# Kernel tuning notes

Hardware: AMD Instinct MI355X
Metric: run time of the kernel (lower is better)

Reference implementation:

```python
import jax, jax.numpy as jnp
import numpy as np

HIDDEN = 2048
NUM_HEADS = 32
NUM_KV_HEADS = 8
HEAD_DIM = 128
EPS = 1e-6
ROPE_BASE = 10000.0
T = 2048


def setup_inputs() -> dict:
    key = jax.random.key(0)
    k1, k2, k3, k4, k5 = jax.random.split(key, 5)
    q_size = NUM_HEADS * HEAD_DIM
    kv_size = NUM_KV_HEADS * HEAD_DIM
    s = 0.02
    return {
        "positions": jnp.arange(T, dtype=jnp.int32),
        "hidden_states": jax.random.normal(k1, (T, HIDDEN), dtype=jnp.float32),
        "wqkv": jax.random.normal(k2, (q_size + 2 * kv_size, HIDDEN), dtype=jnp.float32) * s,
        "wo": jax.random.normal(k3, (HIDDEN, q_size), dtype=jnp.float32) * s,
        "q_norm_w": jnp.ones((HEAD_DIM,), dtype=jnp.float32),
        "k_norm_w": jnp.ones((HEAD_DIM,), dtype=jnp.float32),
    }


def _rms_norm(x, w, eps=EPS):
    # x: [T, H, D]; normalize over last dim
    var = jnp.mean(jnp.square(x), axis=-1, keepdims=True)
    return x * jax.lax.rsqrt(var + eps) * w


def _rope(positions, x):
    # neox-style rotate-half RoPE. x: [T, H, D]
    half = HEAD_DIM // 2
    inv_freq = 1.0 / (ROPE_BASE ** (jnp.arange(0, half, dtype=jnp.float32) / half))
    ang = positions.astype(jnp.float32)[:, None] * inv_freq  # [T, half]
    cos = jnp.cos(ang)[:, None, :]  # [T, 1, half]
    sin = jnp.sin(ang)[:, None, :]
    x1, x2 = x[..., :half], x[..., half:]
    return jnp.concatenate([x1 * cos - x2 * sin, x2 * cos + x1 * sin], axis=-1)


def reference(positions, hidden_states, wqkv, wo, q_norm_w, k_norm_w):
    q_size = NUM_HEADS * HEAD_DIM
    kv_size = NUM_KV_HEADS * HEAD_DIM
    scaling = HEAD_DIM ** -0.5

    qkv = hidden_states @ wqkv.T  # [T, q_size + 2*kv_size]
    q = qkv[:, :q_size].reshape(-1, NUM_HEADS, HEAD_DIM)
    k = qkv[:, q_size:q_size + kv_size].reshape(-1, NUM_KV_HEADS, HEAD_DIM)
    v = qkv[:, q_size + kv_size:].reshape(-1, NUM_KV_HEADS, HEAD_DIM)

    q = _rms_norm(q, q_norm_w)
    k = _rms_norm(k, k_norm_w)
    q = _rope(positions, q)
    k = _rope(positions, k)

    # GQA: repeat kv heads to match query heads
    group = NUM_HEADS // NUM_KV_HEADS
    k = jnp.repeat(k, group, axis=1)  # [T, H, D]
    v = jnp.repeat(v, group, axis=1)

    scores = jnp.einsum("thd,shd->hts", q, k) * scaling  # [H, T, T]
    causal = positions[:, None] >= positions[None, :]  # [T, T]
    scores = jnp.where(causal[None], scores, jnp.finfo(scores.dtype).min)
    probs = jax.nn.softmax(scores, axis=-1)
    o = jnp.einsum("hts,shd->thd", probs, v)  # [T, H, D]
    return o.reshape(-1, q_size) @ wo.T  # [T, HIDDEN]
```

## Files before the change

### kernel.cpp

```cpp
#include <hip/hip_runtime.h>
#include <hip/hip_bf16.h>

#define T_SEQ   2048
#define HIDDEN  2048
#define NUM_H   32
#define NUM_KV  8
#define HD      128
#define Q_SIZE  4096
#define QKV_N   6144

typedef __bf16 bf16;
typedef __bf16 bf16x8 __attribute__((ext_vector_type(8)));
typedef __bf16 bf16x4 __attribute__((ext_vector_type(4)));
typedef float  floatx4 __attribute__((ext_vector_type(4)));

#define GLOBAL_AS(p) ((const __attribute__((address_space(1))) void*)(p))
#define LDS_AS(p)    ((__attribute__((address_space(3))) void*)(p))

#define BARRIER() do { asm volatile("" ::: "memory"); \
                       __builtin_amdgcn_s_barrier();  \
                       asm volatile("" ::: "memory"); } while (0)
#define VMCNT(n) asm volatile("s_waitcnt vmcnt(" #n ")" ::: "memory")

__global__ void detect_dtype(const unsigned short* __restrict__ wq, int* flagp)
{
    const int lane = threadIdx.x;
    int cnt = 0;
    for (int i = lane; i < 512; i += 64) {
        int ef = (wq[i] >> 7) & 0xFF;
        if (ef >= 90 && ef <= 130) cnt++;
    }
    #pragma unroll
    for (int m = 32; m; m >>= 1) cnt += __shfl_xor(cnt, m);
    if (lane == 0) *flagp = (cnt >= 430) ? 1 : 0;
}

__global__ __launch_bounds__(256) void convert_all(
    const void* __restrict__ h, const void* __restrict__ wq,
    const void* __restrict__ wo_, const void* __restrict__ qn,
    const void* __restrict__ kn,
    bf16* __restrict__ hb, bf16* __restrict__ wqb, bf16* __restrict__ wob,
    bf16* __restrict__ qnb, bf16* __restrict__ knb, const int* flagp)
{
    long e = ((long)blockIdx.x * 256 + threadIdx.x) * 8;
    const void* src; bf16* dst; long off;
    if      (e < 4194304)  { src = h;   dst = hb;  off = e; }
    else if (e < 16777216) { src = wq;  dst = wqb; off = e - 4194304; }
    else if (e < 25165824) { src = wo_; dst = wob; off = e - 16777216; }
    else if (e < 25165952) { src = qn;  dst = qnb; off = e - 25165824; }
    else if (e < 25166080) { src = kn;  dst = knb; off = e - 25165952; }
    else return;

    if (*flagp) {
        *(bf16x8*)(dst + off) = *(const bf16x8*)((const bf16*)src + off);
    } else {
        const float* f = (const float*)src + off;
        bf16x8 v;
        #pragma unroll
        for (int i = 0; i < 8; ++i) v[i] = (bf16)f[i];
        *(bf16x8*)(dst + off) = v;
    }
}

__global__ __launch_bounds__(512, 2) void gemm8p(
    const bf16* __restrict__ A, const bf16* __restrict__ B,
    bf16* __restrict__ C, int N, int K, int lda, int ldb)
{
    __shared__ bf16 As[2][2][128 * 64];
    __shared__ bf16 Bs[2][192 * 64];

    const int tid  = threadIdx.x;
    const int wave = tid >> 6, lane = tid & 63;
    const int quad = lane >> 4, l16 = lane & 15;
    const int wm = wave >> 2;
    const int wn = wave & 3;
    const long baseN = (long)blockIdx.x * 192;
    const long baseM = (long)blockIdx.y * 256;

    const int sr  = tid >> 3;
    const int sgc = ((tid & 7) ^ (sr & 7)) * 8;

    auto stagePA = [&](int p, int g, int t) {
        const long kc = (long)t * 64;
        const bf16* src = A + (baseM + g * 64 + sr) * (long)lda + kc + sgc;
        __builtin_amdgcn_global_load_lds(GLOBAL_AS(src),
            LDS_AS(&As[p][0][g * 4096 + wave * 512]), 16, 0, 0);
        __builtin_amdgcn_global_load_lds(GLOBAL_AS(src + 128 * (long)lda),
            LDS_AS(&As[p][1][g * 4096 + wave * 512]), 16, 0, 0);
    };
    auto stagePBu = [&](int p, int u, int t) {
        const long kc = (long)t * 64;
        const bf16* src = B + (baseN + u * 64 + sr) * (long)ldb + kc + sgc;
        __builtin_amdgcn_global_load_lds(GLOBAL_AS(src),
            LDS_AS(&Bs[p][u * 4096 + wave * 512]), 16, 0, 0);
    };

    floatx4 acc[8][3] = {};
    bf16x8 af[4][2], bf01[2][2], bf2[2];

    auto rdAf = [&](int p, int g) {
        #pragma unroll
        for (int mf = 0; mf < 4; ++mf)
            #pragma unroll
            for (int ks = 0; ks < 2; ++ks) {
                const int r = g * 64 + mf * 16 + l16;
                af[mf][ks] = *(const bf16x8*)(&As[p][wm][r * 64 + (((ks * 4 + quad) ^ (r & 7)) * 8)]);
            }
    };
    auto rdB01 = [&](int p) {
        #pragma unroll
        for (int nf = 0; nf < 2; ++nf)
            #pragma unroll
            for (int ks = 0; ks < 2; ++ks) {
                const int r = wn * 48 + nf * 16 + l16;
                bf01[nf][ks] = *(const bf16x8*)(&Bs[p][r * 64 + (((ks * 4 + quad) ^ (r & 7)) * 8)]);
            }
    };
    auto rdB2 = [&](int p) {
        #pragma unroll
        for (int ks = 0; ks < 2; ++ks) {
            const int r = wn * 48 + 32 + l16;
            bf2[ks] = *(const bf16x8*)(&Bs[p][r * 64 + (((ks * 4 + quad) ^ (r & 7)) * 8)]);
        }
    };
    auto mmQ2 = [&](int mo) {
        __builtin_amdgcn_s_setprio(1);
        #pragma unroll
        for (int mf = 0; mf < 4; ++mf)
            #pragma unroll
            for (int nf = 0; nf < 2; ++nf)
                #pragma unroll
                for (int ks = 0; ks < 2; ++ks)
                    acc[mo + mf][nf] = __builtin_amdgcn_mfma_f32_16x16x32_bf16(
                        af[mf][ks], bf01[nf][ks], acc[mo + mf][nf], 0, 0, 0);
        __builtin_amdgcn_s_setprio(0);
    };
    auto mmQ1 = [&](int mo) {
        __builtin_amdgcn_s_setprio(1);
        #pragma unroll
        for (int mf = 0; mf < 4; ++mf)
            #pragma unroll
            for (int ks = 0; ks < 2; ++ks)
                acc[mo + mf][2] = __builtin_amdgcn_mfma_f32_16x16x32_bf16(
                    af[mf][ks], bf2[ks], acc[mo + mf][2], 0, 0, 0);
        __builtin_amdgcn_s_setprio(0);
    };

    stagePBu(0, 0, 0); stagePBu(0, 1, 0); stagePBu(0, 2, 0);
    stagePA(0, 0, 0);  stagePA(0, 1, 0);
    stagePBu(1, 0, 1);
    VMCNT(1);
    BARRIER();

    const int NT2 = K / 128;
    for (int j = 0; j < NT2; ++j) {
        const int t1 = 2 * j + 1;
        const bool more = (j + 1 < NT2);

        rdAf(0, 0); rdB01(0);
        stagePBu(1, 1, t1); stagePBu(1, 2, t1);
        BARRIER(); __builtin_amdgcn_sched_barrier(0);
        mmQ2(0);
        BARRIER();

        rdB2(0);
        stagePA(1, 0, t1);
        VMCNT(5);
        BARRIER(); __builtin_amdgcn_sched_barrier(0);
        mmQ1(0);
        BARRIER();

        rdAf(0, 1);
        stagePA(1, 1, t1);
        BARRIER(); __builtin_amdgcn_sched_barrier(0);
        mmQ2(4);
        BARRIER();

        if (more) { stagePBu(0, 0, t1 + 1); VMCNT(3); } else { VMCNT(2); }
        BARRIER(); __builtin_amdgcn_sched_barrier(0);
        mmQ1(4);
        BARRIER();

        rdAf(1, 0); rdB01(1);
        if (more) { stagePBu(0, 1, t1 + 1); stagePBu(0, 2, t1 + 1); }
        BARRIER(); __builtin_amdgcn_sched_barrier(0);
        mmQ2(0);
        BARRIER();

        rdB2(1);
        if (more) { stagePA(0, 0, t1 + 1); VMCNT(5); } else { VMCNT(0); }
        BARRIER(); __builtin_amdgcn_sched_barrier(0);
        mmQ1(0);
        BARRIER();

        rdAf(1, 1);
        if (more) stagePA(0, 1, t1 + 1);
        BARRIER(); __builtin_amdgcn_sched_barrier(0);
        mmQ2(4);
        BARRIER();

        if (more) { stagePBu(1, 0, t1 + 2); VMCNT(3); }
        BARRIER(); __builtin_amdgcn_sched_barrier(0);
        mmQ1(4);
        BARRIER();
    }

    #pragma unroll
    for (int i = 0; i < 8; ++i)
        #pragma unroll
        for (int j = 0; j < 3; ++j)
            #pragma unroll
            for (int r = 0; r < 4; ++r) {
                long row = baseM + wm * 128 + i * 16 + quad * 4 + r;
                long col = baseN + wn * 48 + j * 16 + l16;
                C[row * (long)N + col] = (bf16)acc[i][j][r];
            }
}

__global__ __launch_bounds__(256, 2) void gemm_db64(
    const bf16* __restrict__ A, const bf16* __restrict__ B,
    float* __restrict__ Cp, int N, int Kd, int lda, int ldb)
{
    __shared__ bf16 As[2][128 * 64];
    __shared__ bf16 Bs[2][128 * 64];

    const int tid  = threadIdx.x;
    const int wave = tid >> 6, lane = tid & 63;
    const int quad = lane >> 4, l16 = lane & 15;
    const int wm = (wave & 1) * 64, wn = (wave >> 1) * 64;
    const long baseM = (long)blockIdx.x * 128;
    const long baseN = (long)blockIdx.y * 128;
    const long koff  = (long)blockIdx.z * Kd;

    const int sr  = tid >> 3;
    const int sgc = ((tid & 7) ^ (sr & 7)) * 8;

    auto stage = [&](int p, int t) {
        const long kc = koff + (long)t * 64;
        #pragma unroll
        for (int u = 0; u < 4; ++u) {
            const bf16* sa = A + (baseM + u * 32 + sr) * (long)lda + kc + sgc;
            __builtin_amdgcn_global_load_lds(GLOBAL_AS(sa),
                LDS_AS(&As[p][u * 2048 + wave * 512]), 16, 0, 0);
        }
        #pragma unroll
        for (int u = 0; u < 4; ++u) {
            const bf16* sb = B + (baseN + u * 32 + sr) * (long)ldb + kc + sgc;
            __builtin_amdgcn_global_load_lds(GLOBAL_AS(sb),
                LDS_AS(&Bs[p][u * 2048 + wave * 512]), 16, 0, 0);
        }
    };

    floatx4 acc[4][4] = {};

    stage(0, 0);

    const int NT = Kd / 64;
    int cur = 0;
    for (int t = 0; t < NT; ++t) {
        if (t + 1 < NT) { stage(cur ^ 1, t + 1); VMCNT(8); }
        else            { VMCNT(0); }
        BARRIER();

        bf16x8 af[4][2], bfr[4][2];
        #pragma unroll
        for (int i = 0; i < 4; ++i)
            #pragma unroll
            for (int ks = 0; ks < 2; ++ks) {
                const int r = wm + i * 16 + l16;
                af[i][ks] = *(const bf16x8*)(&As[cur][r * 64 + (((ks * 4 + quad) ^ (r & 7)) * 8)]);
            }
        #pragma unroll
        for (int j = 0; j < 4; ++j)
            #pragma unroll
            for (int ks = 0; ks < 2; ++ks) {
                const int r = wn + j * 16 + l16;
                bfr[j][ks] = *(const bf16x8*)(&Bs[cur][r * 64 + (((ks * 4 + quad) ^ (r & 7)) * 8)]);
            }

        __builtin_amdgcn_s_setprio(1);
        #pragma unroll
        for (int i = 0; i < 4; ++i)
            #pragma unroll
            for (int j = 0; j < 4; ++j)
                #pragma unroll
                for (int ks = 0; ks < 2; ++ks)
                    acc[i][j] = __builtin_amdgcn_mfma_f32_16x16x32_bf16(
                        af[i][ks], bfr[j][ks], acc[i][j], 0, 0, 0);
        __builtin_amdgcn_s_setprio(0);

        BARRIER();
        cur ^= 1;
    }

    const long Mrows = (long)gridDim.x * 128;
    float* C = Cp + (long)blockIdx.z * Mrows * N;
    #pragma unroll
    for (int i = 0; i < 4; ++i)
        #pragma unroll
        for (int j = 0; j < 4; ++j)
            #pragma unroll
            for (int r = 0; r < 4; ++r) {
                long row = baseM + wm + i * 16 + quad * 4 + r;
                long col = baseN + wn + j * 16 + l16;
                C[row * (long)N + col] = acc[i][j][r];
            }
}

__global__ __launch_bounds__(256) void reduce2(
    const float* __restrict__ P0, const float* __restrict__ P1,
    void* __restrict__ out, const int* flagp)
{
    long i = ((long)blockIdx.x * 256 + threadIdx.x) * 4;
    floatx4 a = *(const floatx4*)(P0 + i);
    floatx4 b = *(const floatx4*)(P1 + i);
    floatx4 s = a + b;
    if (*flagp) {
        bf16x4 o;
        #pragma unroll
        for (int r = 0; r < 4; ++r) o[r] = (bf16)s[r];
        *(bf16x4*)((bf16*)out + i) = o;
    } else {
        *(floatx4*)((float*)out + i) = s;
    }
}

__global__ __launch_bounds__(256) void qkv_post(
    bf16* __restrict__ qkv, const int* __restrict__ positions,
    const bf16* __restrict__ qnw, const bf16* __restrict__ knw)
{
    const int t = blockIdx.x;
    const int tid = threadIdx.x, wave = tid >> 6, lane = tid & 63;
    const float pos = (float)positions[t];

    const float inv = expf(-(float)lane * (float)(9.210340371976184 / 64.0));
    float sn, cs;
    sincosf(pos * inv, &sn, &cs);

    bf16* row = qkv + (long)t * QKV_N;

    for (int u = wave; u < 40; u += 4) {
        bf16* p       = (u < 32) ? row + u * HD : row + Q_SIZE + (u - 32) * HD;
        const bf16* w = (u < 32) ? qnw : knw;
        float x1 = (float)p[lane], x2 = (float)p[lane + 64];
        float ss = x1 * x1 + x2 * x2;
        #pragma unroll
        for (int m = 32; m; m >>= 1) ss += __shfl_xor(ss, m);
        float rr = rsqrtf(ss * (1.f / 128.f) + 1e-6f);
        float y1 = x1 * rr * (float)w[lane];
        float y2 = x2 * rr * (float)w[lane + 64];
        p[lane]      = (bf16)(y1 * cs - y2 * sn);
        p[lane + 64] = (bf16)(y2 * cs + y1 * sn);
    }
}

__global__ __launch_bounds__(256) void vtrans(const bf16* __restrict__ qkv,
                                              bf16* __restrict__ vt)
{
    __shared__ bf16 tile[64][136];
    const int t0 = blockIdx.x * 64, kvh = blockIdx.y, tid = threadIdx.x;

    const int rl = tid >> 4, c8 = (tid & 15) * 8;
    const bf16* src = qkv + (long)t0 * QKV_N + 5120 + kvh * HD;
    #pragma unroll
    for (int it = 0; it < 4; ++it) {
        int r = it * 16 + rl;
        *(bf16x8*)(&tile[r][c8]) = *(const bf16x8*)(src + (long)r * QKV_N + c8);
    }
    __syncthreads();

    const int d = tid >> 1, tb = (tid & 1) * 32;
    bf16* dst = vt + ((long)kvh * HD + d) * T_SEQ + t0 + tb;
    #pragma unroll
    for (int it = 0; it < 4; ++it) {
        bf16x8 v;
        #pragma unroll
        for (int j = 0; j < 8; ++j) v[j] = tile[tb + it * 8 + j][d];
        *(bf16x8*)(dst + it * 8) = v;
    }
}

__global__ __launch_bounds__(256, 3) void attn5(bf16* qkv, const bf16* __restrict__ vt)
{
    __shared__ bf16 Ks[2][64 * 128];
    __shared__ bf16 Vs[128 * 64];

    const int tid  = threadIdx.x, wave = tid >> 6, lane = tid & 63;
    const int quad = lane >> 4, l16 = lane & 15;
    const int h = blockIdx.x, kvh = h >> 2;
    const int iq = 31 - blockIdx.y;
    const int q0 = iq * 64;

    const float C1 = 0.12753236f;
    const float C2 = 17.312340f;

    bf16x8 qf[4];
    {
        const bf16* qa = qkv + (long)(q0 + wave * 16 + l16) * QKV_N + h * HD + quad * 8;
        #pragma unroll
        for (int ks = 0; ks < 4; ++ks) qf[ks] = *(const bf16x8*)(qa + ks * 32);
    }

    floatx4 oacc[8] = {};
    float ls = 0.f;

    const int krl = lane >> 4, kc = lane & 15;
    const int vrl = lane >> 3, vc = lane & 7;
    const int kswz = (kc ^ (wave * 4 + krl)) * 8;
    const int vswz = (vc ^ (vrl & 7)) * 8;
    const int wsig = ((wave & 1) << 1) | (wave >> 1);
    const int sq4  = (((quad & 1) << 1) | (quad >> 1)) << 2;

    const bf16* kg0 = qkv + Q_SIZE + kvh * HD;
    const bf16* vg0 = vt + (long)kvh * HD * T_SEQ;

    auto stageK = [&](int p, int kt) {
        const bf16* kg = kg0 + (long)(kt * 64) * QKV_N;
        #pragma unroll
        for (int it = 0; it < 4; ++it) {
            const int rK = it * 16 + wsig * 4 + krl;
            __builtin_amdgcn_global_load_lds(GLOBAL_AS(kg + (long)rK * QKV_N + kswz),
                                             LDS_AS(&Ks[p][it * 2048 + wave * 512]), 16, 0, 0);
        }
    };
    auto stageV = [&](int kt) {
        const bf16* vg = vg0 + kt * 64;
        #pragma unroll
        for (int it = 0; it < 4; ++it) {
            const int dV = it * 32 + wave * 8 + vrl;
            __builtin_amdgcn_global_load_lds(GLOBAL_AS(vg + (long)dV * T_SEQ + vswz),
                                             LDS_AS(&Vs[it * 2048 + wave * 512]), 16, 0, 0);
        }
    };

    stageK(0, 0);

    const int qg = q0 + wave * 16 + l16;

    for (int kt = 0; kt <= iq; ++kt) {
        const int p = kt & 1;
        __syncthreads();
        stageV(kt);
        if (kt < iq) stageK(p ^ 1, kt + 1);

        const int k0 = kt * 64;

        floatx4 sT[4] = {};
        #pragma unroll
        for (int j2 = 0; j2 < 4; ++j2)
            #pragma unroll
            for (int ks = 0; ks < 4; ++ks) {
                bf16x8 kf = *(const bf16x8*)(&Ks[p][(j2 * 16 + l16) * 128 + (((ks * 4 + quad) ^ l16) * 8)]);
                sT[j2] = __builtin_amdgcn_mfma_f32_16x16x32_bf16(kf, qf[ks], sT[j2], 0, 0, 0);
            }

        const bool diag = (kt == iq);
        unsigned lov[4], hiv[4];
        #pragma unroll
        for (int j2 = 0; j2 < 4; ++j2) {
            float ev[4];
            #pragma unroll
            for (int r = 0; r < 4; ++r) {
                float x = __builtin_amdgcn_exp2f(sT[j2][r] * C1 - C2);
                if (diag && (k0 + j2 * 16 + sq4 + r > qg)) x = 0.f;
                ls += x;
                ev[r] = x;
            }
            asm("v_cvt_pk_bf16_f32 %0, %1, %2" : "=v"(lov[j2]) : "v"(ev[0]), "v"(ev[1]));
            asm("v_cvt_pk_bf16_f32 %0, %1, %2" : "=v"(hiv[j2]) : "v"(ev[2]), "v"(ev[3]));
        }

        bf16x8 pa[2];
        #pragma unroll
        for (int ks2 = 0; ks2 < 2; ++ks2) {
            auto wl = __builtin_amdgcn_permlane32_swap(lov[2 * ks2], lov[2 * ks2 + 1], false, false);
            auto wh = __builtin_amdgcn_permlane32_swap(hiv[2 * ks2], hiv[2 * ks2 + 1], false, false);
            union { unsigned w[4]; bf16x8 v; } u;
            u.w[0] = wl[0]; u.w[1] = wh[0]; u.w[2] = wl[1]; u.w[3] = wh[1];
            pa[ks2] = u.v;
        }

        if (kt < iq) asm volatile("s_waitcnt vmcnt(4)" ::: "memory");
        else         asm volatile("s_waitcnt vmcnt(0)" ::: "memory");
        __builtin_amdgcn_s_barrier();
        __builtin_amdgcn_sched_barrier(0);

        #pragma unroll
        for (int ks2 = 0; ks2 < 2; ++ks2)
            #pragma unroll
            for (int vj = 0; vj < 8; ++vj) {
                const int d = vj * 16 + l16;
                bf16x8 vb = *(const bf16x8*)(&Vs[d * 64 + (((ks2 * 4 + quad) ^ (d & 7)) * 8)]);
                oacc[vj] = __builtin_amdgcn_mfma_f32_16x16x32_bf16(pa[ks2], vb, oacc[vj], 0, 0, 0);
            }
    }

    ls += __shfl_xor(ls, 16); ls += __shfl_xor(ls, 32);
    float rinv[4];
    #pragma unroll
    for (int r = 0; r < 4; ++r) rinv[r] = 1.f / __shfl(ls, quad * 4 + r);

    #pragma unroll
    for (int vj = 0; vj < 8; ++vj)
        #pragma unroll
        for (int r = 0; r < 4; ++r) {
            const long row = q0 + wave * 16 + quad * 4 + r;
            qkv[row * (long)QKV_N + h * HD + vj * 16 + l16] = (bf16)(oacc[vj][r] * rinv[r]);
        }
}

extern "C" void kernel_launch(void* const* d_in, const int* in_sizes, int n_in,
                              void* d_out, int out_size, void* d_ws, size_t ws_size,
                              hipStream_t stream)
{
    const int* positions = (const int*)d_in[0];

    char* ws = (char*)d_ws;
    bf16* qkv  = (bf16*)(ws);
    bf16* hb   = (bf16*)(ws + 25165824);
    bf16* vt   = hb;
    float* P0  = (float*)(ws + 25165824);
    float* P1  = (float*)(ws + 41943040);
    bf16* wqb  = (bf16*)(ws + 33554432);
    bf16* wob  = (bf16*)(ws + 58720256);
    bf16* qnb  = (bf16*)(ws + 75497472);
    bf16* knb  = (bf16*)(ws + 75497728);
    int*  flag = (int*) (ws + 75497984);

    detect_dtype<<<dim3(1), dim3(64), 0, stream>>>((const unsigned short*)d_in[2], flag);
    convert_all<<<dim3(12289), dim3(256), 0, stream>>>(
        d_in[1], d_in[2], d_in[3], d_in[4], d_in[5],
        hb, wqb, wob, qnb, knb, flag);

    gemm8p<<<dim3(QKV_N / 192, T_SEQ / 256), dim3(512), 0, stream>>>(
        hb, wqb, qkv, QKV_N, HIDDEN, HIDDEN, HIDDEN);
    vtrans<<<dim3(T_SEQ / 64, NUM_KV), dim3(256), 0, stream>>>(qkv, vt);
    qkv_post<<<dim3(T_SEQ), dim3(256), 0, stream>>>(qkv, positions, qnb, knb);
    attn5<<<dim3(NUM_H, 32), dim3(256), 0, stream>>>(qkv, vt);
    gemm_db64<<<dim3(T_SEQ / 128, HIDDEN / 128, 2), dim3(256), 0, stream>>>(
        qkv, wob, P0, HIDDEN, Q_SIZE / 2, QKV_N, Q_SIZE);
    reduce2<<<dim3(4096), dim3(256), 0, stream>>>(P0, P1, d_out, flag);
}
```

Baseline: 308.2 us.

## Restructure QKV GEMM main loop from 8-phase to 3-phase pipeline

Rewrites the QKV projection GEMM's inner loop so each 64-wide K tile runs in three compute phases instead of eight interleaved phases per 128 K. Both A-fragment halves are kept in registers, and prefetches of the next tile are issued at phase boundaries. The goal is fewer barriers and less per-phase synchronization overhead. The cost is higher register pressure from the extra A fragments and coarser overlap between loads and MFMA work, and the wait counts were re-derived by hand.

```diff
diff --git a/kernel.cpp b/kernel.cpp
--- a/kernel.cpp
+++ b/kernel.cpp
@@ -21,6 +21,7 @@
                        __builtin_amdgcn_s_barrier();  \
                        asm volatile("" ::: "memory"); } while (0)
 #define VMCNT(n) asm volatile("s_waitcnt vmcnt(" #n ")" ::: "memory")
+#define SCHED()  __builtin_amdgcn_sched_barrier(0)
 
 __global__ void detect_dtype(const unsigned short* __restrict__ wq, int* flagp)
 {
@@ -62,7 +63,7 @@
     }
 }
 
-__global__ __launch_bounds__(512, 2) void gemm8p(
+__global__ __launch_bounds__(512, 2) void gemm3p(
     const bf16* __restrict__ A, const bf16* __restrict__ B,
     bf16* __restrict__ C, int N, int K, int lda, int ldb)
 {
@@ -96,15 +97,24 @@
     };
 
     floatx4 acc[8][3] = {};
-    bf16x8 af[4][2], bf01[2][2], bf2[2];
-
-    auto rdAf = [&](int p, int g) {
+    bf16x8 af0[4][2], af1[4][2], bf01[2][2], bf2[2];
+
+    auto rdAf0 = [&](int p) {
         #pragma unroll
         for (int mf = 0; mf < 4; ++mf)
             #pragma unroll
             for (int ks = 0; ks < 2; ++ks) {
-                const int r = g * 64 + mf * 16 + l16;
-                af[mf][ks] = *(const bf16x8*)(&As[p][wm][r * 64 + (((ks * 4 + quad) ^ (r & 7)) * 8)]);
+                const int r = mf * 16 + l16;
+                af0[mf][ks] = *(const bf16x8*)(&As[p][wm][r * 64 + (((ks * 4 + quad) ^ (r & 7)) * 8)]);
+            }
+    };
+    auto rdAf1 = [&](int p) {
+        #pragma unroll
+        for (int mf = 0; mf < 4; ++mf)
+            #pragma unroll
+            for (int ks = 0; ks < 2; ++ks) {
+                const int r = 64 + mf * 16 + l16;
+                af1[mf][ks] = *(const bf16x8*)(&As[p][wm][r * 64 + (((ks * 4 + quad) ^ (r & 7)) * 8)]);
             }
     };
     auto rdB01 = [&](int p) {
@@ -123,7 +133,8 @@
             bf2[ks] = *(const bf16x8*)(&Bs[p][r * 64 + (((ks * 4 + quad) ^ (r & 7)) * 8)]);
         }
     };
-    auto mmQ2 = [&](int mo) {
+
+    auto mmA0B01 = [&]() {
         __builtin_amdgcn_s_setprio(1);
         #pragma unroll
         for (int mf = 0; mf < 4; ++mf)
@@ -131,77 +142,69 @@
             for (int nf = 0; nf < 2; ++nf)
                 #pragma unroll
                 for (int ks = 0; ks < 2; ++ks)
-                    acc[mo + mf][nf] = __builtin_amdgcn_mfma_f32_16x16x32_bf16(
-                        af[mf][ks], bf01[nf][ks], acc[mo + mf][nf], 0, 0, 0);
+                    acc[mf][nf] = __builtin_amdgcn_mfma_f32_16x16x32_bf16(
+                        af0[mf][ks], bf01[nf][ks], acc[mf][nf], 0, 0, 0);
         __builtin_amdgcn_s_setprio(0);
     };
-    auto mmQ1 = [&](int mo) {
+    auto mmB2 = [&]() {
         __builtin_amdgcn_s_setprio(1);
         #pragma unroll
         for (int mf = 0; mf < 4; ++mf)
             #pragma unroll
             for (int ks = 0; ks < 2; ++ks)
-                acc[mo + mf][2] = __builtin_amdgcn_mfma_f32_16x16x32_bf16(
-                    af[mf][ks], bf2[ks], acc[mo + mf][2], 0, 0, 0);
+                acc[mf][2] = __builtin_amdgcn_mfma_f32_16x16x32_bf16(
+                    af0[mf][ks], bf2[ks], acc[mf][2], 0, 0, 0);
+        #pragma unroll
+        for (int mf = 0; mf < 4; ++mf)
+            #pragma unroll
+            for (int ks = 0; ks < 2; ++ks)
+                acc[4 + mf][2] = __builtin_amdgcn_mfma_f32_16x16x32_bf16(
+                    af1[mf][ks], bf2[ks], acc[4 + mf][2], 0, 0, 0);
+        __builtin_amdgcn_s_setprio(0);
+    };
+    auto mmA1B01 = [&]() {
+        __builtin_amdgcn_s_setprio(1);
+        #pragma unroll
+        for (int mf = 0; mf < 4; ++mf)
+            #pragma unroll
+            for (int nf = 0; nf < 2; ++nf)
+                #pragma unroll
+                for (int ks = 0; ks < 2; ++ks)
+                    acc[4 + mf][nf] = __builtin_amdgcn_mfma_f32_16x16x32_bf16(
+                        af1[mf][ks], bf01[nf][ks], acc[4 + mf][nf], 0, 0, 0);
         __builtin_amdgcn_s_setprio(0);
     };
 
     stagePBu(0, 0, 0); stagePBu(0, 1, 0); stagePBu(0, 2, 0);
     stagePA(0, 0, 0);  stagePA(0, 1, 0);
-    stagePBu(1, 0, 1);
-    VMCNT(1);
+    VMCNT(2);
     BARRIER();
 
-    const int NT2 = K / 128;
-    for (int j = 0; j < NT2; ++j) {
-        const int t1 = 2 * j + 1;
-        const bool more = (j + 1 < NT2);
-
-        rdAf(0, 0); rdB01(0);
-        stagePBu(1, 1, t1); stagePBu(1, 2, t1);
-        BARRIER(); __builtin_amdgcn_sched_barrier(0);
-        mmQ2(0);
+    const int NT = K / 64;
+    for (int t = 0; t < NT; ++t) {
+        const int p = t & 1;
+        const bool more = (t + 1 < NT);
+
+        rdAf0(p); rdB01(p); rdB2(p);
+        if (more) {
+            stagePBu(p ^ 1, 0, t + 1); stagePBu(p ^ 1, 1, t + 1); stagePBu(p ^ 1, 2, t + 1);
+            VMCNT(3);
+        } else {
+            VMCNT(0);
+        }
+        BARRIER(); SCHED();
+        mmA0B01();
         BARRIER();
 
-        rdB2(0);
-        stagePA(1, 0, t1);
-        VMCNT(5);
-        BARRIER(); __builtin_amdgcn_sched_barrier(0);
-        mmQ1(0);
+        rdAf1(p);
+        if (more) stagePA(p ^ 1, 0, t + 1);
+        BARRIER(); SCHED();
+        mmB2();
         BARRIER();
 
-        rdAf(0, 1);
-        stagePA(1, 1, t1);
-        BARRIER(); __builtin_amdgcn_sched_barrier(0);
-        mmQ2(4);
-        BARRIER();
-
-        if (more) { stagePBu(0, 0, t1 + 1); VMCNT(3); } else { VMCNT(2); }
-        BARRIER(); __builtin_amdgcn_sched_barrier(0);
-        mmQ1(4);
-        BARRIER();
-
-        rdAf(1, 0); rdB01(1);
-        if (more) { stagePBu(0, 1, t1 + 1); stagePBu(0, 2, t1 + 1); }
-        BARRIER(); __builtin_amdgcn_sched_barrier(0);
-        mmQ2(0);
-        BARRIER();
-
-        rdB2(1);
-        if (more) { stagePA(0, 0, t1 + 1); VMCNT(5); } else { VMCNT(0); }
-        BARRIER(); __builtin_amdgcn_sched_barrier(0);
-        mmQ1(0);
-        BARRIER();
-
-        rdAf(1, 1);
-        if (more) stagePA(0, 1, t1 + 1);
-        BARRIER(); __builtin_amdgcn_sched_barrier(0);
-        mmQ2(4);
-        BARRIER();
-
-        if (more) { stagePBu(1, 0, t1 + 2); VMCNT(3); }
-        BARRIER(); __builtin_amdgcn_sched_barrier(0);
-        mmQ1(4);
+        if (more) { stagePA(p ^ 1, 1, t + 1); VMCNT(2); }
+        SCHED();
+        mmA1B01();
         BARRIER();
     }
 
@@ -532,7 +535,7 @@
         d_in[1], d_in[2], d_in[3], d_in[4], d_in[5],
         hb, wqb, wob, qnb, knb, flag);
 
-    gemm8p<<<dim3(QKV_N / 192, T_SEQ / 256), dim3(512), 0, stream>>>(
+    gemm3p<<<dim3(QKV_N / 192, T_SEQ / 256), dim3(512), 0, stream>>>(
         hb, wqb, qkv, QKV_N, HIDDEN, HIDDEN, HIDDEN);
     vtrans<<<dim3(T_SEQ / 64, NUM_KV), dim3(256), 0, stream>>>(qkv, vt);
     qkv_post<<<dim3(T_SEQ), dim3(256), 0, stream>>>(qkv, positions, qnb, knb);
```

Measured after the change: 306.3 us. No clear change (-0.6%).
